# Kernel tuning notes

Hardware: AMD Instinct MI355X
Metric: run time of the kernel (lower is better)

Reference implementation:

```python
import jax, jax.numpy as jnp
import numpy as np

N_QUBITS = 8
DEPTH = 3


def _apply_1q(state, U, q):
    # state: (2,)*n complex, apply 2x2 unitary U on qubit axis q
    state = jnp.moveaxis(state, q, -1)
    state = state @ U.T
    return jnp.moveaxis(state, -1, q)


def _ry(state, theta, q):
    h = theta * 0.5
    c, s = jnp.cos(h), jnp.sin(h)
    U = jnp.stack([jnp.stack([c, -s]), jnp.stack([s, c])]).astype(jnp.complex64)
    return _apply_1q(state, U, q)


def _rz(state, theta, q):
    h = theta * 0.5
    d = jnp.stack([jnp.exp(-1j * h), jnp.exp(1j * h)]).astype(jnp.complex64)
    state = jnp.moveaxis(state, q, -1) * d
    return jnp.moveaxis(state, -1, q)


def _cx(state, c, t):
    # CNOT with control c, target t: flip target amplitudes where control=1
    state = jnp.moveaxis(state, (c, t), (-2, -1))
    s0 = state[..., 0, :]
    s1 = state[..., 1, ::-1]
    state = jnp.stack([s0, s1], axis=-2)
    return jnp.moveaxis(state, (-2, -1), (c, t))


def _simulate(angles, qparams):
    # Single-sample circuit: RY angle encoding, then DEPTH layers of (RZ,RY) per
    # qubit + CX ring. Returns <Z_0> (Hamiltonian 'Z' + 'I'*(n-1)).
    state = jnp.zeros((2,) * N_QUBITS, jnp.complex64).at[(0,) * N_QUBITS].set(1.0)
    for q in range(N_QUBITS):
        state = _ry(state, angles[q], q)
    idx = 0
    for _ in range(DEPTH):
        for q in range(N_QUBITS):
            state = _rz(state, qparams[idx], q); idx += 1
            state = _ry(state, qparams[idx], q); idx += 1
        for i in range(N_QUBITS):
            state = _cx(state, i, (i + 1) % N_QUBITS)
    probs = jnp.abs(state) ** 2
    return probs[0].sum() - probs[1].sum()


def setup_inputs() -> dict:
    key = jax.random.key(0)
    ks = jax.random.split(key, 6)
    B, F, H = 16384, 16, 256
    nq = 2 * N_QUBITS * DEPTH  # 48 variational params
    return {
        "x": jax.random.normal(ks[0], (B, F), jnp.float32),
        "enc_w1": jax.random.normal(ks[1], (H, F), jnp.float32) / np.sqrt(F).astype(np.float32),
        "enc_b1": jnp.zeros((H,), jnp.float32),
        "enc_w2": jax.random.normal(ks[2], (N_QUBITS, H), jnp.float32) / np.sqrt(H).astype(np.float32),
        "enc_b2": jnp.zeros((N_QUBITS,), jnp.float32),
        "qparams": jax.random.normal(ks[3], (nq,), jnp.float32) * 0.1,
        "dec_w1": jax.random.normal(ks[4], (H, 1), jnp.float32),
        "dec_b1": jnp.zeros((H,), jnp.float32),
        "dec_w2": jax.random.normal(ks[5], (1, H), jnp.float32) / np.sqrt(H).astype(np.float32),
        "dec_b2": jnp.zeros((1,), jnp.float32),
    }


def reference(x, enc_w1, enc_b1, enc_w2, enc_b2, qparams, dec_w1, dec_b1, dec_w2, dec_b2):
    # encoder: Linear -> ReLU -> Linear -> Tanh, scaled by pi (angle encoding)
    h = jax.nn.relu(x @ enc_w1.T + enc_b1)
    angles = jnp.tanh(h @ enc_w2.T + enc_b2) * jnp.pi  # (B, n_qubits)
    # vectorized quantum state-vector simulation over the batch
    expvals = jax.vmap(_simulate, in_axes=(0, None))(angles, qparams)  # (B,)
    q = expvals[:, None]  # (B, 1)
    # decoder: Linear(1->H) -> ReLU -> Linear(H->1) -> Sigmoid
    d = jax.nn.relu(q @ dec_w1.T + dec_b1)
    return jax.nn.sigmoid(d @ dec_w2.T + dec_b2)
```

## Files before the change

kernel.cpp:

```cpp
#include <hip/hip_runtime.h>
#include <math.h>

#define NQ 8
#define DEPTH 3
#define FDIM 16
#define HDIM 256
#define WAVES_PER_BLOCK 4
#define THREADS (WAVES_PER_BLOCK * 64)
#define ROWS_PER_BLOCK (WAVES_PER_BLOCK * 2)
#define NGATE (NQ * DEPTH)

template<int CTRL>
__device__ __forceinline__ float dpp1(float v) {
    return __int_as_float(__builtin_amdgcn_update_dpp(
        0, __float_as_int(v), CTRL, 0xF, 0xF, true));
}

template<int M4>
__device__ __forceinline__ float shuf4(float v) {
    if constexpr (M4 == 1)  return dpp1<0xB1>(v);
    else if constexpr (M4 == 2)  return dpp1<0x4E>(v);
    else if constexpr (M4 == 4)  return dpp1<0x1B>(dpp1<0x141>(v));
    else if constexpr (M4 == 8)  return dpp1<0x128>(v);
    else return v;
}

template<int ML>
__device__ __forceinline__ float shuf(float v, int lane) {
    if constexpr (ML == 0) {
        return v;
    } else if constexpr (ML >= 32) {
        int addr = (lane ^ ML) << 2;
        return __int_as_float(__builtin_amdgcn_ds_bpermute(addr, __float_as_int(v)));
    } else {
        return __int_as_float(__builtin_amdgcn_ds_swizzle(
            __float_as_int(v), (ML << 10) | 0x1F));
    }
}

__device__ __forceinline__ float wred(float v, int lane) {
    v += shuf4<1>(v);
    v += shuf4<2>(v);
    v += shuf4<4>(v);
    v += shuf4<8>(v);
#if __has_builtin(__builtin_amdgcn_permlane16_swap)
    {
        auto r = __builtin_amdgcn_permlane16_swap(__float_as_int(v), __float_as_int(v), false, false);
        v = __int_as_float(r[0]) + __int_as_float(r[1]);
    }
#else
    v += __shfl_xor(v, 16, 64);
#endif
#if __has_builtin(__builtin_amdgcn_permlane32_swap)
    {
        auto r = __builtin_amdgcn_permlane32_swap(__float_as_int(v), __float_as_int(v), false, false);
        v = __int_as_float(r[0]) + __int_as_float(r[1]);
    }
#else
    v += __shfl_xor(v, 32, 64);
#endif
    return v;
}

__device__ __forceinline__ float fast_tanh(float y) {
    float ex = __expf(2.f * y);
    return 1.f - 2.f * __builtin_amdgcn_rcpf(ex + 1.f);
}

template<int M, int R>
__device__ __forceinline__ void gate2x2(float (&srA)[4], float (&siA)[4],
                                        float (&srB)[4], float (&siB)[4],
                                        float cz, float szv, float cy, float sy,
                                        int lane) {
    constexpr int ML = M & 63, MH = (M >> 6) & 3;
    constexpr int RL = R & 63, RH = (R >> 6) & 3;
    bool p0;
    if constexpr (RL == 0)                 p0 = false;
    else if constexpr ((RL & (RL-1)) == 0) p0 = (lane & RL) != 0;
    else                                   p0 = (__popc(lane & RL) & 1) != 0;
    float sgz = p0 ? szv : -szv;
    float sgy = p0 ? sy  : -sy;
#pragma unroll
    for (int hi = 0; hi < 4; hi++) {
        const bool f = (__builtin_popcount(hi & RH) & 1) != 0;
        float z = f ? -sgz : sgz;
        float nrA = fmaf(srA[hi], cz, -(siA[hi] * z));
        float niA = fmaf(siA[hi], cz,  (srA[hi] * z));
        srA[hi] = nrA; siA[hi] = niA;
        float nrB = fmaf(srB[hi], cz, -(siB[hi] * z));
        float niB = fmaf(siB[hi], cz,  (srB[hi] * z));
        srB[hi] = nrB; siB[hi] = niB;
    }
    float prA[4], piA[4], prB[4], piB[4];
#pragma unroll
    for (int hi = 0; hi < 4; hi++) {
        prA[hi] = shuf<ML>(srA[hi ^ MH], lane);
        piA[hi] = shuf<ML>(siA[hi ^ MH], lane);
        prB[hi] = shuf<ML>(srB[hi ^ MH], lane);
        piB[hi] = shuf<ML>(siB[hi ^ MH], lane);
    }
#pragma unroll
    for (int hi = 0; hi < 4; hi++) {
        const bool f = (__builtin_popcount(hi & RH) & 1) != 0;
        float yv = f ? -sgy : sgy;
        srA[hi] = fmaf(yv, prA[hi], cy * srA[hi]);
        siA[hi] = fmaf(yv, piA[hi], cy * siA[hi]);
        srB[hi] = fmaf(yv, prB[hi], cy * srB[hi]);
        siB[hi] = fmaf(yv, piB[hi], cy * siB[hi]);
    }
}

__global__ __launch_bounds__(THREADS, 8) void hqcl_kernel(
    const float* __restrict__ x,
    const float* __restrict__ w1,
    const float* __restrict__ b1,
    const float* __restrict__ w2,
    const float* __restrict__ b2,
    const float* __restrict__ qp,
    const float* __restrict__ dw1,
    const float* __restrict__ db1,
    const float* __restrict__ dw2,
    const float* __restrict__ db2,
    float* __restrict__ out, int B)
{
    __shared__ float4 sG4[NGATE];

    const int t = threadIdx.x;
    if (t < 2 * NGATE) {
        float s, c;
        __sincosf(qp[t] * 0.5f, &s, &c);
        float* p = (float*)&sG4[t >> 1] + 2 * (t & 1);
        p[0] = c; p[1] = s;
    }
    __syncthreads();

    const int lane = t & 63;
    const int row0 = blockIdx.x * ROWS_PER_BLOCK + (t >> 6) * 2;
    if (row0 >= B) return;

    const float4* xA = (const float4*)(x + row0 * FDIM);
    const float4* xB = (const float4*)(x + (row0 + 1) * FDIM);
    float4 xa0 = xA[0], xa1 = xA[1], xa2 = xA[2], xa3 = xA[3];
    float4 xb0 = xB[0], xb1 = xB[1], xb2 = xB[2], xb3 = xB[3];

    float hA[4], hB[4];
#pragma unroll
    for (int m = 0; m < 4; m++) {
        int j = lane + 64 * m;
        const float4* wp = (const float4*)(w1 + j * FDIM);
        float4 wa = wp[0], wb = wp[1], wc = wp[2], wd = wp[3];
        float bv = b1[j];
        float aA = bv, aB = bv;
        aA = fmaf(xa0.x, wa.x, aA); aA = fmaf(xa0.y, wa.y, aA);
        aA = fmaf(xa0.z, wa.z, aA); aA = fmaf(xa0.w, wa.w, aA);
        aA = fmaf(xa1.x, wb.x, aA); aA = fmaf(xa1.y, wb.y, aA);
        aA = fmaf(xa1.z, wb.z, aA); aA = fmaf(xa1.w, wb.w, aA);
        aA = fmaf(xa2.x, wc.x, aA); aA = fmaf(xa2.y, wc.y, aA);
        aA = fmaf(xa2.z, wc.z, aA); aA = fmaf(xa2.w, wc.w, aA);
        aA = fmaf(xa3.x, wd.x, aA); aA = fmaf(xa3.y, wd.y, aA);
        aA = fmaf(xa3.z, wd.z, aA); aA = fmaf(xa3.w, wd.w, aA);
        aB = fmaf(xb0.x, wa.x, aB); aB = fmaf(xb0.y, wa.y, aB);
        aB = fmaf(xb0.z, wa.z, aB); aB = fmaf(xb0.w, wa.w, aB);
        aB = fmaf(xb1.x, wb.x, aB); aB = fmaf(xb1.y, wb.y, aB);
        aB = fmaf(xb1.z, wb.z, aB); aB = fmaf(xb1.w, wb.w, aB);
        aB = fmaf(xb2.x, wc.x, aB); aB = fmaf(xb2.y, wc.y, aB);
        aB = fmaf(xb2.z, wc.z, aB); aB = fmaf(xb2.w, wc.w, aB);
        aB = fmaf(xb3.x, wd.x, aB); aB = fmaf(xb3.y, wd.y, aB);
        aB = fmaf(xb3.z, wd.z, aB); aB = fmaf(xb3.w, wd.w, aB);
        hA[m] = fmaxf(aA, 0.f);
        hB[m] = fmaxf(aB, 0.f);
    }

    float c0A[NQ], s0A[NQ], c0B[NQ], s0B[NQ];
#pragma unroll
    for (int q = 0; q < NQ; q++) {
        float aA = 0.f, aB = 0.f;
#pragma unroll
        for (int m = 0; m < 4; m++) {
            float wv = w2[q * HDIM + lane + 64 * m];
            aA = fmaf(hA[m], wv, aA);
            aB = fmaf(hB[m], wv, aB);
        }
        aA = wred(aA, lane);
        aB = wred(aB, lane);
        float bq = b2[q];
        float uA = 0.25f * fast_tanh(aA + bq);
        float uB = 0.25f * fast_tanh(aB + bq);
        float svA, cvA, svB, cvB;
        asm("v_sin_f32 %0, %1" : "=v"(svA) : "v"(uA));
        asm("v_cos_f32 %0, %1" : "=v"(cvA) : "v"(uA));
        asm("v_sin_f32 %0, %1" : "=v"(svB) : "v"(uB));
        asm("v_cos_f32 %0, %1" : "=v"(cvB) : "v"(uB));
        s0A[q] = svA; c0A[q] = cvA;
        s0B[q] = svB; c0B[q] = cvB;
    }

    float plA = 1.f, plB = 1.f;
#pragma unroll
    for (int b = 0; b < 6; b++) {
        int q = 7 - b;
        bool bit = (lane >> b) & 1;
        plA *= bit ? s0A[q] : c0A[q];
        plB *= bit ? s0B[q] : c0B[q];
    }
    float srA[4], siA[4], srB[4], siB[4];
    srA[0] = plA * c0A[1] * c0A[0];
    srA[1] = plA * s0A[1] * c0A[0];
    srA[2] = plA * c0A[1] * s0A[0];
    srA[3] = plA * s0A[1] * s0A[0];
    srB[0] = plB * c0B[1] * c0B[0];
    srB[1] = plB * s0B[1] * c0B[0];
    srB[2] = plB * c0B[1] * s0B[0];
    srB[3] = plB * s0B[1] * s0B[0];
#pragma unroll
    for (int hi = 0; hi < 4; hi++) { siA[hi] = 0.f; siB[hi] = 0.f; }

#define GATE(L, Q, MM, RR) { float4 g4 = sG4[(L)*8 + (Q)]; \
        gate2x2<MM, RR>(srA, siA, srB, siB, g4.x, g4.y, g4.z, g4.w, lane); }
    GATE(0,0,0x80,0x80) GATE(0,1,0x40,0x40) GATE(0,2,0x20,0x20) GATE(0,3,0x10,0x10)
    GATE(0,4,0x08,0x08) GATE(0,5,0x04,0x04) GATE(0,6,0x02,0x02) GATE(0,7,0x01,0x01)
    GATE(1,0,0xC0,0x7F) GATE(1,1,0x60,0xC0) GATE(1,2,0x30,0xE0) GATE(1,3,0x18,0xF0)
    GATE(1,4,0x0C,0xF8) GATE(1,5,0x06,0xFC) GATE(1,6,0x03,0xFE) GATE(1,7,0xC1,0xFF)
    GATE(2,0,0xA0,0xD5) GATE(2,1,0x50,0xBF) GATE(2,2,0x28,0x5F) GATE(2,3,0x14,0xAF)
    GATE(2,4,0x0A,0x57) GATE(2,5,0x05,0xAB) GATE(2,6,0xC2,0x55) GATE(2,7,0x61,0xAA)
#undef GATE

    bool pb = (__popc(lane & 0x0C) & 1) != 0;
    float m0A = srA[0]*srA[0] + siA[0]*siA[0] + srA[2]*srA[2] + siA[2]*siA[2];
    float m1A = srA[1]*srA[1] + siA[1]*siA[1] + srA[3]*srA[3] + siA[3]*siA[3];
    float m0B = srB[0]*srB[0] + siB[0]*siB[0] + srB[2]*srB[2] + siB[2]*siB[2];
    float m1B = srB[1]*srB[1] + siB[1]*siB[1] + srB[3]*srB[3] + siB[3]*siB[3];
    float eA = pb ? (m1A - m0A) : (m0A - m1A);
    float eB = pb ? (m1B - m0B) : (m0B - m1B);
    eA = wred(eA, lane);
    eB = wred(eB, lane);

    float accA = 0.f, accB = 0.f;
#pragma unroll
    for (int m = 0; m < 4; m++) {
        int j = lane + 64 * m;
        float w1v = dw1[j], bv = db1[j], w2v = dw2[j];
        float dA = fmaxf(fmaf(eA, w1v, bv), 0.f);
        float dB = fmaxf(fmaf(eB, w1v, bv), 0.f);
        accA = fmaf(dA, w2v, accA);
        accB = fmaf(dB, w2v, accB);
    }
    accA = wred(accA, lane);
    accB = wred(accB, lane);
    if (lane == 0) {
        float bb = db2[0];
        out[row0] = 1.f / (1.f + __expf(-(accA + bb)));
        if (row0 + 1 < B)
            out[row0 + 1] = 1.f / (1.f + __expf(-(accB + bb)));
    }
}

extern "C" void kernel_launch(void* const* d_in, const int* in_sizes, int n_in,
                              void* d_out, int out_size, void* d_ws, size_t ws_size,
                              hipStream_t stream) {
    const float* x   = (const float*)d_in[0];
    const float* w1  = (const float*)d_in[1];
    const float* b1  = (const float*)d_in[2];
    const float* w2  = (const float*)d_in[3];
    const float* b2  = (const float*)d_in[4];
    const float* qp  = (const float*)d_in[5];
    const float* dw1 = (const float*)d_in[6];
    const float* db1 = (const float*)d_in[7];
    const float* dw2 = (const float*)d_in[8];
    const float* db2 = (const float*)d_in[9];
    float* out = (float*)d_out;

    const int B = in_sizes[0] / FDIM;
    const int grid = (B + ROWS_PER_BLOCK - 1) / ROWS_PER_BLOCK;
    hqcl_kernel<<<grid, THREADS, 0, stream>>>(x, w1, b1, w2, b2, qp, dw1, db1, dw2, db2, out, B);
}
```

Before: 39.85 us.

## Fuse RZ and RY into one precomputed 2x2 gate matrix applied after shuffle

Precomputes the product RY·RZ per gate in shared memory as four real coefficients (cz*cy, sz*cy, cz*sy, sz*sy), so each gate does the shuffle first and then one fused complex update instead of a separate RZ phase pass followed by an RY mix. It also computes the initial product state inline while the angles are produced, rather than keeping arrays of cos/sin, which lowers register pressure. The launch-bounds occupancy hint drops from 8 to 4 and the second row index is clamped for odd B. The fused update uses slightly more FMAs per element but removes a dependent pass and the sign selects.

```diff
diff --git a/kernel.cpp b/kernel.cpp
--- a/kernel.cpp
+++ b/kernel.cpp
@@ -68,29 +68,17 @@
 }
 
 template<int M, int R>
-__device__ __forceinline__ void gate2x2(float (&srA)[4], float (&siA)[4],
-                                        float (&srB)[4], float (&siB)[4],
-                                        float cz, float szv, float cy, float sy,
-                                        int lane) {
+__device__ __forceinline__ void gate_m(float (&srA)[4], float (&siA)[4],
+                                       float (&srB)[4], float (&siB)[4],
+                                       float a0, float a1, float b0, float b1,
+                                       int lane) {
     constexpr int ML = M & 63, MH = (M >> 6) & 3;
     constexpr int RL = R & 63, RH = (R >> 6) & 3;
     bool p0;
     if constexpr (RL == 0)                 p0 = false;
     else if constexpr ((RL & (RL-1)) == 0) p0 = (lane & RL) != 0;
     else                                   p0 = (__popc(lane & RL) & 1) != 0;
-    float sgz = p0 ? szv : -szv;
-    float sgy = p0 ? sy  : -sy;
-#pragma unroll
-    for (int hi = 0; hi < 4; hi++) {
-        const bool f = (__builtin_popcount(hi & RH) & 1) != 0;
-        float z = f ? -sgz : sgz;
-        float nrA = fmaf(srA[hi], cz, -(siA[hi] * z));
-        float niA = fmaf(siA[hi], cz,  (srA[hi] * z));
-        srA[hi] = nrA; siA[hi] = niA;
-        float nrB = fmaf(srB[hi], cz, -(siB[hi] * z));
-        float niB = fmaf(siB[hi], cz,  (srB[hi] * z));
-        srB[hi] = nrB; siB[hi] = niB;
-    }
+
     float prA[4], piA[4], prB[4], piB[4];
 #pragma unroll
     for (int hi = 0; hi < 4; hi++) {
@@ -99,18 +87,27 @@
         prB[hi] = shuf<ML>(srB[hi ^ MH], lane);
         piB[hi] = shuf<ML>(siB[hi ^ MH], lane);
     }
+
+    float ea1 = p0 ? a1 : -a1;
+    float eb0 = p0 ? b0 : -b0;
+
 #pragma unroll
     for (int hi = 0; hi < 4; hi++) {
         const bool f = (__builtin_popcount(hi & RH) & 1) != 0;
-        float yv = f ? -sgy : sgy;
-        srA[hi] = fmaf(yv, prA[hi], cy * srA[hi]);
-        siA[hi] = fmaf(yv, piA[hi], cy * siA[hi]);
-        srB[hi] = fmaf(yv, prB[hi], cy * srB[hi]);
-        siB[hi] = fmaf(yv, piB[hi], cy * siB[hi]);
-    }
-}
-
-__global__ __launch_bounds__(THREADS, 8) void hqcl_kernel(
+        float za1 = f ? -ea1 : ea1;
+        float zb0 = f ? -eb0 : eb0;
+        float lrA = fmaf(-za1, siA[hi], a0 * srA[hi]);
+        float liA = fmaf( za1, srA[hi], a0 * siA[hi]);
+        srA[hi] = fmaf( b1, piA[hi], fmaf(zb0, prA[hi], lrA));
+        siA[hi] = fmaf(-b1, prA[hi], fmaf(zb0, piA[hi], liA));
+        float lrB = fmaf(-za1, siB[hi], a0 * srB[hi]);
+        float liB = fmaf( za1, srB[hi], a0 * siB[hi]);
+        srB[hi] = fmaf( b1, piB[hi], fmaf(zb0, prB[hi], lrB));
+        siB[hi] = fmaf(-b1, prB[hi], fmaf(zb0, piB[hi], liB));
+    }
+}
+
+__global__ __launch_bounds__(THREADS, 4) void hqcl_kernel(
     const float* __restrict__ x,
     const float* __restrict__ w1,
     const float* __restrict__ b1,
@@ -126,20 +123,21 @@
     __shared__ float4 sG4[NGATE];
 
     const int t = threadIdx.x;
-    if (t < 2 * NGATE) {
-        float s, c;
-        __sincosf(qp[t] * 0.5f, &s, &c);
-        float* p = (float*)&sG4[t >> 1] + 2 * (t & 1);
-        p[0] = c; p[1] = s;
+    if (t < NGATE) {
+        float cz, sz, cy, sy;
+        __sincosf(qp[2 * t] * 0.5f,     &sz, &cz);
+        __sincosf(qp[2 * t + 1] * 0.5f, &sy, &cy);
+        sG4[t] = make_float4(cz * cy, sz * cy, cz * sy, sz * sy);
     }
     __syncthreads();
 
     const int lane = t & 63;
     const int row0 = blockIdx.x * ROWS_PER_BLOCK + (t >> 6) * 2;
     if (row0 >= B) return;
+    const int rowB = (row0 + 1 < B) ? row0 + 1 : row0;
 
     const float4* xA = (const float4*)(x + row0 * FDIM);
-    const float4* xB = (const float4*)(x + (row0 + 1) * FDIM);
+    const float4* xB = (const float4*)(x + rowB * FDIM);
     float4 xa0 = xA[0], xa1 = xA[1], xa2 = xA[2], xa3 = xA[3];
     float4 xb0 = xB[0], xb1 = xB[1], xb2 = xB[2], xb3 = xB[3];
 
@@ -171,7 +169,8 @@
         hB[m] = fmaxf(aB, 0.f);
     }
 
-    float c0A[NQ], s0A[NQ], c0B[NQ], s0B[NQ];
+    float c0A, s0A, c1A, s1A, c0B, s0B, c1B, s1B;
+    float plA = 1.f, plB = 1.f;
 #pragma unroll
     for (int q = 0; q < NQ; q++) {
         float aA = 0.f, aB = 0.f;
@@ -191,32 +190,25 @@
         asm("v_cos_f32 %0, %1" : "=v"(cvA) : "v"(uA));
         asm("v_sin_f32 %0, %1" : "=v"(svB) : "v"(uB));
         asm("v_cos_f32 %0, %1" : "=v"(cvB) : "v"(uB));
-        s0A[q] = svA; c0A[q] = cvA;
-        s0B[q] = svB; c0B[q] = cvB;
-    }
-
-    float plA = 1.f, plB = 1.f;
-#pragma unroll
-    for (int b = 0; b < 6; b++) {
-        int q = 7 - b;
-        bool bit = (lane >> b) & 1;
-        plA *= bit ? s0A[q] : c0A[q];
-        plB *= bit ? s0B[q] : c0B[q];
-    }
+        if (q == 0)      { c0A = cvA; s0A = svA; c0B = cvB; s0B = svB; }
+        else if (q == 1) { c1A = cvA; s1A = svA; c1B = cvB; s1B = svB; }
+        else {
+            bool bit = (lane >> (7 - q)) & 1;
+            plA *= bit ? svA : cvA;
+            plB *= bit ? svB : cvB;
+        }
+    }
+
     float srA[4], siA[4], srB[4], siB[4];
-    srA[0] = plA * c0A[1] * c0A[0];
-    srA[1] = plA * s0A[1] * c0A[0];
-    srA[2] = plA * c0A[1] * s0A[0];
-    srA[3] = plA * s0A[1] * s0A[0];
-    srB[0] = plB * c0B[1] * c0B[0];
-    srB[1] = plB * s0B[1] * c0B[0];
-    srB[2] = plB * c0B[1] * s0B[0];
-    srB[3] = plB * s0B[1] * s0B[0];
+    srA[0] = plA * c1A * c0A;  srA[1] = plA * s1A * c0A;
+    srA[2] = plA * c1A * s0A;  srA[3] = plA * s1A * s0A;
+    srB[0] = plB * c1B * c0B;  srB[1] = plB * s1B * c0B;
+    srB[2] = plB * c1B * s0B;  srB[3] = plB * s1B * s0B;
 #pragma unroll
     for (int hi = 0; hi < 4; hi++) { siA[hi] = 0.f; siB[hi] = 0.f; }
 
 #define GATE(L, Q, MM, RR) { float4 g4 = sG4[(L)*8 + (Q)]; \
-        gate2x2<MM, RR>(srA, siA, srB, siB, g4.x, g4.y, g4.z, g4.w, lane); }
+        gate_m<MM, RR>(srA, siA, srB, siB, g4.x, g4.y, g4.z, g4.w, lane); }
     GATE(0,0,0x80,0x80) GATE(0,1,0x40,0x40) GATE(0,2,0x20,0x20) GATE(0,3,0x10,0x10)
     GATE(0,4,0x08,0x08) GATE(0,5,0x04,0x04) GATE(0,6,0x02,0x02) GATE(0,7,0x01,0x01)
     GATE(1,0,0xC0,0x7F) GATE(1,1,0x60,0xC0) GATE(1,2,0x30,0xE0) GATE(1,3,0x18,0xF0)
```

New measurement: 39.22 us. About the same (-1.6%).
